# Kernel optimization log

Measured on AMD Instinct MI355X. Metric: run time of the kernel, lower is better.

Reference implementation:

```python
import jax, jax.numpy as jnp
import numpy as np

B, S, C, H = 64, 512, 256, 128
P = S  # predict_length defaults to seq_length


def _linear_init(k, fan_in, fan_out):
    bound = 1.0 / np.sqrt(fan_in)
    kw, kb = jax.random.split(k)
    w = jax.random.uniform(kw, (fan_in, fan_out), minval=-bound, maxval=bound, dtype=jnp.float32)
    b = jax.random.uniform(kb, (fan_out,), minval=-bound, maxval=bound, dtype=jnp.float32)
    return w, b


def setup_inputs() -> dict:
    key = jax.random.key(0)
    ks = jax.random.split(key, 10)
    x = jax.random.normal(ks[0], (B, S, C), dtype=jnp.float32)
    wq1, bq1 = _linear_init(ks[1], S, H)
    wk1, bk1 = _linear_init(ks[2], S, H)
    wq2, bq2 = _linear_init(ks[3], S // 2, H)
    wk2, bk2 = _linear_init(ks[4], S // 2, H)
    wq3, bq3 = _linear_init(ks[5], S // 4, H)
    wk3, bk3 = _linear_init(ks[6], S // 4, H)
    wv, bv = _linear_init(ks[7], S, S)
    wo, bo = _linear_init(ks[8], S, P)
    return dict(x=x, wq1=wq1, bq1=bq1, wk1=wk1, bk1=bk1,
                wq2=wq2, bq2=bq2, wk2=wk2, bk2=bk2,
                wq3=wq3, bq3=bq3, wk3=wk3, bk3=bk3,
                wv=wv, bv=bv, wo=wo, bo=bo)


def _channel_attn(xl, wq, bq, wk, bk):
    # xl: [b', C, L]; q,k: [b', C, H]; returns softmax channel-attention [b', C, C]
    q = xl @ wq + bq
    k = xl @ wk + bk
    scores = jnp.einsum('bch,bdh->bcd', q, k) / jnp.sqrt(jnp.asarray(H, q.dtype))
    return jax.nn.softmax(scores, axis=-1)


def reference(x, wq1, bq1, wk1, bk1, wq2, bq2, wk2, bk2, wq3, bq3, wk3, bk3, wv, bv, wo, bo):
    b, s, c = x.shape
    x1 = jnp.swapaxes(x, -2, -1)                                   # [B, C, S]
    x2 = jnp.swapaxes(x.reshape(b * 2, s // 2, c), -2, -1)          # [2B, C, S/2]
    x3 = jnp.swapaxes(x.reshape(b * 4, s // 4, c), -2, -1)          # [4B, C, S/4]
    a1 = _channel_attn(x1, wq1, bq1, wk1, bk1)                      # [B, C, C]
    a2 = _channel_attn(x2, wq2, bq2, wk2, bk2).reshape(b, 2, c, c).mean(axis=1)
    a3 = _channel_attn(x3, wq3, bq3, wk3, bk3).reshape(b, 4, c, c).mean(axis=1)
    stacked = jnp.stack([a1, a2, a3], axis=0)                       # [3, B, C, C]
    gate = jax.nn.softmax(stacked, axis=0)                          # softmax over scales
    attn = (stacked * gate).sum(axis=0)                             # gated multi-scale combine [B, C, C]
    v = x1 @ wv + bv                                                # [B, C, S]
    out = (attn @ v) @ wo + bo                                      # [B, C, P]
    return jnp.swapaxes(out, -2, -1)                                # [B, P, C]
```

## Files before the change

### kernel.cpp

```cpp
#include <hip/hip_runtime.h>
#include <hip/hip_bf16.h>


typedef __attribute__((ext_vector_type(8))) short bf16x8;
typedef __attribute__((ext_vector_type(4))) float f32x4;
typedef __attribute__((ext_vector_type(8))) unsigned short ushort8;
typedef __attribute__((ext_vector_type(4))) unsigned int uint4v;

typedef __attribute__((address_space(1))) void* as1vp;
typedef __attribute__((address_space(3))) void* as3vp;

__device__ __forceinline__ void gl2lds16(const void* g, void* l) {
  __builtin_amdgcn_global_load_lds((as1vp)(void*)g, (as3vp)l, 16, 0, 0);
}

__device__ __forceinline__ float bf2f(unsigned short u) {
  union { unsigned int i; float f; } v; v.i = ((unsigned int)u) << 16; return v.f;
}
__device__ __forceinline__ unsigned short f2bf(float f) {
  union { float f; unsigned int i; } v; v.f = f;
  unsigned int r = v.i + 0x7FFFu + ((v.i >> 16) & 1u);
  return (unsigned short)(r >> 16);
}
__device__ __forceinline__ unsigned int cvtpk(float a, float b) {
  unsigned int r;
  asm("v_cvt_pk_bf16_f32 %0, %1, %2" : "=v"(r) : "v"(a), "v"(b));
  return r;
}
__device__ __forceinline__ unsigned long long pack4pk(float a, float b, float c, float d) {
  return (unsigned long long)cvtpk(a, b) | ((unsigned long long)cvtpk(c, d) << 32);
}

__global__ void __launch_bounds__(256) tcast_all(
    const float* __restrict__ x,
    const float* __restrict__ wq1, const float* __restrict__ wk1,
    const float* __restrict__ wq2, const float* __restrict__ wk2,
    const float* __restrict__ wq3, const float* __restrict__ wk3,
    const float* __restrict__ wv, const float* __restrict__ wo,
    unsigned short* __restrict__ XT,
    unsigned short* __restrict__ W1, unsigned short* __restrict__ W2,
    unsigned short* __restrict__ W3, unsigned short* __restrict__ WVNT,
    unsigned short* __restrict__ WOT) {
  const int bid = blockIdx.x;
  const int t = threadIdx.x;
  if (bid >= 2168) {
    long i0 = (long)(bid - 2168) * 2048 + t * 8;
    f32x4 a = *(const f32x4*)(wv + i0);
    f32x4 b = *(const f32x4*)(wv + i0 + 4);
    uint4v o = {cvtpk(a[0], a[1]), cvtpk(a[2], a[3]), cvtpk(b[0], b[1]), cvtpk(b[2], b[3])};
    *(uint4v*)(WVNT + i0) = o;
    return;
  }
  __shared__ float lds[64][68];
  const float* S; unsigned short* D; int R, Cc, r0, c0, rowoff = 0;
  if (bid < 2048) {
    int bz = bid >> 5, i = bid & 31;
    S = x + (long)bz * 131072; D = XT + (long)bz * 131072;
    R = 512; Cc = 256; r0 = (i & 7) * 64; c0 = (i >> 3) * 64;
  } else {
    int wb = bid - 2048;
    if (wb < 32) {
      int m = wb >> 4, i = wb & 15;
      S = m ? wk1 : wq1; D = W1; R = 512; Cc = 128;
      r0 = (i & 7) * 64; c0 = (i >> 3) * 64; rowoff = m * 128;
    } else if (wb < 48) {
      int m = (wb - 32) >> 3, i = (wb - 32) & 7;
      S = m ? wk2 : wq2; D = W2; R = 256; Cc = 128;
      r0 = (i & 3) * 64; c0 = (i >> 2) * 64; rowoff = m * 128;
    } else if (wb < 56) {
      int m = (wb - 48) >> 2, i = (wb - 48) & 3;
      S = m ? wk3 : wq3; D = W3; R = 128; Cc = 128;
      r0 = (i & 1) * 64; c0 = (i >> 1) * 64; rowoff = m * 128;
    } else {
      int i = wb - 56; S = wo; D = WOT; R = 512; Cc = 512;
      r0 = (i & 7) * 64; c0 = (i >> 3) * 64;
    }
  }
  {
    const int row = t >> 2, cq = (t & 3) * 16;
    const float* Sp = S + (long)(r0 + row) * Cc + c0 + cq;
#pragma unroll
    for (int j = 0; j < 4; ++j)
      *(f32x4*)&lds[row][cq + j * 4] = *(const f32x4*)(Sp + j * 4);
  }
  __syncthreads();
  {
    const int rq = (t & 15) * 4, ccb = t >> 4;
#pragma unroll
    for (int j = 0; j < 4; ++j) {
      int cc = ccb + j * 16;
      *(unsigned long long*)(D + (long)(c0 + cc + rowoff) * R + r0 + rq) =
          pack4pk(lds[rq][cc], lds[rq + 1][cc], lds[rq + 2][cc], lds[rq + 3][cc]);
    }
  }
}

__global__ void __launch_bounds__(1024) projscore(
    const unsigned short* __restrict__ XT,
    const unsigned short* __restrict__ W1, const unsigned short* __restrict__ W2,
    const unsigned short* __restrict__ W3,
    const unsigned short* __restrict__ WOT, const unsigned short* __restrict__ WVNT,
    unsigned short* __restrict__ WVOT, float* __restrict__ BVO,
    const float* __restrict__ bv,
    unsigned short* __restrict__ A1F, unsigned short* __restrict__ A2F,
    unsigned short* __restrict__ A3F,
    const float* __restrict__ bq1, const float* __restrict__ bk1,
    const float* __restrict__ bq2, const float* __restrict__ bk2,
    const float* __restrict__ bq3, const float* __restrict__ bk3) {
  extern __shared__ char smem[];
  const int z = blockIdx.z;
  const int t = threadIdx.x, lane = t & 63, wid = t >> 6;

  if (z >= 464) {
    int p0 = (z - 464) * 128 + wid * 8;
    f32x4 b0 = *(const f32x4*)(bv + lane * 8);
    f32x4 b1 = *(const f32x4*)(bv + lane * 8 + 4);
#pragma unroll
    for (int i = 0; i < 8; ++i) {
      int p = p0 + i;
      bf16x8 wrow = *(const bf16x8*)(WOT + (long)p * 512 + lane * 8);
      float s = 0.0f;
#pragma unroll
      for (int j = 0; j < 4; ++j) {
        s += b0[j] * bf2f((unsigned short)wrow[j]);
        s += b1[j] * bf2f((unsigned short)wrow[4 + j]);
      }
#pragma unroll
      for (int off = 1; off < 64; off <<= 1) s += __shfl_xor(s, off, 64);
      if (lane == 0) BVO[p] = s;
    }
    return;
  }

  const int rS = t >> 3, sS = t & 7;

  if (z >= 448) {
    const int w = z - 448;
    const int m0 = (w >> 2) * 128, n0 = (w & 3) * 128;
    const unsigned short* Ab = WOT + (long)m0 * 512;
    const unsigned short* Bb = WVNT + (long)n0 * 512;
    const int wmb = (wid >> 2) * 32, wnb = (wid & 3) * 32;
    f32x4 acc[2][2] = {};
    for (int k0 = 0; k0 < 512; k0 += 64) {
      int sc = (sS ^ (rS & 7)) * 8;
      gl2lds16(Ab + (long)rS * 512 + k0 + sc, smem + t * 16);
      gl2lds16(Bb + (long)rS * 512 + k0 + sc, smem + 16384 + t * 16);
      __syncthreads();
#pragma unroll
      for (int kk = 0; kk < 2; ++kk) {
        const int slot = kk * 4 + (lane >> 4);
        bf16x8 af[2], bfr[2];
#pragma unroll
        for (int mi = 0; mi < 2; ++mi) {
          int row = wmb + mi * 16 + (lane & 15);
          af[mi] = *(const bf16x8*)(smem + row * 128 + 16 * (slot ^ (row & 7)));
        }
#pragma unroll
        for (int ni = 0; ni < 2; ++ni) {
          int row = wnb + ni * 16 + (lane & 15);
          bfr[ni] = *(const bf16x8*)(smem + 16384 + row * 128 + 16 * (slot ^ (row & 7)));
        }
#pragma unroll
        for (int mi = 0; mi < 2; ++mi)
#pragma unroll
          for (int ni = 0; ni < 2; ++ni)
            acc[mi][ni] = __builtin_amdgcn_mfma_f32_16x16x32_bf16(af[mi], bfr[ni], acc[mi][ni], 0, 0, 0);
      }
      __syncthreads();
    }
#pragma unroll
    for (int ni = 0; ni < 2; ++ni) {
      int col = n0 + wnb + ni * 16 + (lane & 15);
#pragma unroll
      for (int mi = 0; mi < 2; ++mi) {
        int rowb = m0 + wmb + mi * 16 + (lane >> 4) * 4;
#pragma unroll
        for (int r = 0; r < 4; ++r)
          WVOT[(long)(rowb + r) * 512 + col] = f2bf(acc[mi][ni][r]);
      }
    }
    return;
  }

  const unsigned short* Ab; const unsigned short* Bw; unsigned short* AF;
  const float *bq, *bk; int K; long sb;
  if (z < 64) {
    K = 512; Bw = W1; AF = A1F; sb = z; bq = bq1; bk = bk1;
    Ab = XT + (long)z * 131072;
  } else if (z < 192) {
    int u = z - 64; K = 256; Bw = W2; AF = A2F; sb = u; bq = bq2; bk = bk2;
    Ab = XT + (long)(u >> 1) * 131072 + (u & 1) * 256;
  } else {
    int u = z - 192; K = 128; Bw = W3; AF = A3F; sb = u; bq = bq3; bk = bk3;
    Ab = XT + (long)(u >> 2) * 131072 + (u & 3) * 128;
  }
  const int wmb = (wid >> 2) * 64, wnb = (wid & 3) * 64;

  auto stage = [&](int buf, int k0) {
    char* s = smem + buf * 65536;
#pragma unroll
    for (int i = 0; i < 2; ++i) {
      int row = i * 128 + rS;
      int sc = (sS ^ (row & 7)) * 8;
      gl2lds16(Ab + (long)row * 512 + k0 + sc, s + i * 16384 + t * 16);
      gl2lds16(Bw + (long)row * K + k0 + sc, s + 32768 + i * 16384 + t * 16);
    }
  };

  f32x4 acc[4][4] = {};
  const int nst = K >> 6;
  stage(0, 0);
  __syncthreads();
  int cur = 0;
  for (int j = 0; j < nst; ++j) {
    if (j + 1 < nst) stage(cur ^ 1, (j + 1) * 64);
    const char* s = smem + cur * 65536;
#pragma unroll
    for (int kk = 0; kk < 2; ++kk) {
      const int slot = kk * 4 + (lane >> 4);
      bf16x8 af[4], bfr[4];
#pragma unroll
      for (int mi = 0; mi < 4; ++mi) {
        int row = wmb + mi * 16 + (lane & 15);
        af[mi] = *(const bf16x8*)(s + row * 128 + 16 * (slot ^ (row & 7)));
      }
#pragma unroll
      for (int ni = 0; ni < 4; ++ni) {
        int row = wnb + ni * 16 + (lane & 15);
        bfr[ni] = *(const bf16x8*)(s + 32768 + row * 128 + 16 * (slot ^ (row & 7)));
      }
#pragma unroll
      for (int mi = 0; mi < 4; ++mi)
#pragma unroll
        for (int ni = 0; ni < 4; ++ni)
          acc[mi][ni] = __builtin_amdgcn_mfma_f32_16x16x32_bf16(bfr[ni], af[mi], acc[mi][ni], 0, 0, 0);
    }
    __syncthreads();
    cur ^= 1;
  }

  {
    const int chB = (wnb < 128) ? 0 : 65536;
    const float* bias = (wnb < 128) ? bq : bk;
    const int hbase = wnb & 127;
#pragma unroll
    for (int mi = 0; mi < 4; ++mi) {
      int rowm = wmb + mi * 16 + (lane & 15);
#pragma unroll
      for (int ni = 0; ni < 4; ++ni) {
        int h = hbase + ni * 16 + (lane >> 4) * 4;
        int addr = chB + (h >> 6) * 32768 + rowm * 128 +
                   16 * (((h & 63) >> 3) ^ (rowm & 7)) + (h & 7) * 2;
        *(unsigned long long*)(smem + addr) =
            pack4pk(acc[mi][ni][0] + bias[h], acc[mi][ni][1] + bias[h + 1],
                    acc[mi][ni][2] + bias[h + 2], acc[mi][ni][3] + bias[h + 3]);
      }
    }
  }
  __syncthreads();

  f32x4 acc2[16] = {};
  const int qrow = wid * 16 + (lane & 15);
#pragma unroll
  for (int kc = 0; kc < 2; ++kc)
#pragma unroll
    for (int kk = 0; kk < 2; ++kk) {
      const int slot = kk * 4 + (lane >> 4);
      bf16x8 qf = *(const bf16x8*)(smem + kc * 32768 + qrow * 128 + 16 * (slot ^ (qrow & 7)));
#pragma unroll
      for (int ni = 0; ni < 16; ++ni) {
        int krow = ni * 16 + (lane & 15);
        bf16x8 kf = *(const bf16x8*)(smem + 65536 + kc * 32768 + krow * 128 + 16 * (slot ^ (krow & 7)));
        acc2[ni] = __builtin_amdgcn_mfma_f32_16x16x32_bf16(qf, kf, acc2[ni], 0, 0, 0);
      }
    }

  const float sc = 0.088388347648318447f;
  {
    int m0idx = wid >> 2, quad = wid & 3;
    unsigned short* Of = AF + ((sb * 4 + m0idx) * 256 + quad * 64 + lane) * 64;
#pragma unroll
    for (int r = 0; r < 4; ++r) {
      float mx = -1e30f;
#pragma unroll
      for (int ni = 0; ni < 16; ++ni) mx = fmaxf(mx, acc2[ni][r]);
#pragma unroll
      for (int off = 1; off < 16; off <<= 1) mx = fmaxf(mx, __shfl_xor(mx, off, 64));
      float s = 0.0f;
      float p[16];
#pragma unroll
      for (int ni = 0; ni < 16; ++ni) {
        p[ni] = __expf((acc2[ni][r] - mx) * sc);
        s += p[ni];
      }
#pragma unroll
      for (int off = 1; off < 16; off <<= 1) s += __shfl_xor(s, off, 64);
      float inv = 1.0f / s;
      uint4v wlo = {cvtpk(p[0] * inv, p[1] * inv), cvtpk(p[2] * inv, p[3] * inv),
                    cvtpk(p[4] * inv, p[5] * inv), cvtpk(p[6] * inv, p[7] * inv)};
      uint4v whi = {cvtpk(p[8] * inv, p[9] * inv), cvtpk(p[10] * inv, p[11] * inv),
                    cvtpk(p[12] * inv, p[13] * inv), cvtpk(p[14] * inv, p[15] * inv)};
      *(uint4v*)(Of + r * 16) = wlo;
      *(uint4v*)(Of + r * 16 + 8) = whi;
    }
  }
}

__global__ void __launch_bounds__(256) gate_frag(
    const unsigned short* __restrict__ A1F, const unsigned short* __restrict__ A2F,
    const unsigned short* __restrict__ A3F, unsigned short* __restrict__ ATTN) {
  const long gid = (long)blockIdx.x * 256 + threadIdx.x;
  const long i = gid * 8;
  const int b = (int)(i >> 16);
  const int rest = (int)(i & 65535);
  ushort8 a1 = *(const ushort8*)(A1F + i);
  const long i2 = ((long)(2 * b) << 16) + rest;
  ushort8 a2a = *(const ushort8*)(A2F + i2);
  ushort8 a2b = *(const ushort8*)(A2F + i2 + 65536);
  const long i3 = ((long)(4 * b) << 16) + rest;
  ushort8 a3a = *(const ushort8*)(A3F + i3);
  ushort8 a3b = *(const ushort8*)(A3F + i3 + 65536);
  ushort8 a3c = *(const ushort8*)(A3F + i3 + 131072);
  ushort8 a3d = *(const ushort8*)(A3F + i3 + 196608);
  const int f = rest & 63;
  const int tl = (rest >> 6) & 255;
  const int m0idx = rest >> 14;
  const int quad = (tl >> 6) & 3;
  const int lane_s = tl & 63;
  const int r = f >> 4;
  const int u0 = f & 15;
  const int row = m0idx * 64 + quad * 16 + (lane_s >> 4) * 4 + r;
  unsigned short* Orow = ATTN + ((long)b << 16) + (long)row * 256 + (lane_s & 15);
#pragma unroll
  for (int j = 0; j < 8; ++j) {
    float A1 = bf2f(a1[j]);
    float A2 = 0.5f * (bf2f(a2a[j]) + bf2f(a2b[j]));
    float A3 = 0.25f * (bf2f(a3a[j]) + bf2f(a3b[j]) + bf2f(a3c[j]) + bf2f(a3d[j]));
    float m = fmaxf(A1, fmaxf(A2, A3));
    float e1 = __expf(A1 - m), e2 = __expf(A2 - m), e3 = __expf(A3 - m);
    Orow[(u0 + j) * 16] = f2bf((A1 * e1 + A2 * e2 + A3 * e3) / (e1 + e2 + e3));
  }
}

template <int F32OUT, int BIASMODE>
__global__ void __launch_bounds__(512) gemm8(
    const unsigned short* __restrict__ A, const unsigned short* __restrict__ B,
    void* __restrict__ OutV, const float* __restrict__ bias,
    int lda, int ldb, int K, long astr, long bstr, long ostr, int ldo) {
  extern __shared__ char smem[];
  const int t = threadIdx.x, lane = t & 63, wid = t >> 6;
  const int wmb = (wid >> 1) * 64, wnb = (wid & 1) * 64;
  const int m0 = blockIdx.y * 256, n0 = blockIdx.x * 128;
  const int bz = blockIdx.z;
  const unsigned short* Ab = A + (long)bz * astr + (long)m0 * lda;
  const unsigned short* Bb = B + (long)bz * bstr + (long)n0 * ldb;
  const int srow = t >> 3, ssl = t & 7;

  auto stage = [&](int buf, int k0) {
    char* s = smem + buf * 49152;
#pragma unroll
    for (int i = 0; i < 4; ++i) {
      int row = i * 64 + srow;
      gl2lds16(Ab + (long)row * lda + k0 + (ssl ^ (row & 7)) * 8, s + i * 8192 + t * 16);
    }
#pragma unroll
    for (int i = 0; i < 2; ++i) {
      int row = i * 64 + srow;
      gl2lds16(Bb + (long)row * ldb + k0 + (ssl ^ (row & 7)) * 8,
               s + 32768 + i * 8192 + t * 16);
    }
  };

  f32x4 acc[4][4] = {};
  const int nst = K >> 6;
  stage(0, 0);
  stage(1, 64);
  for (int j = 0; j < nst; ++j) {
    if (j + 1 < nst) asm volatile("s_waitcnt vmcnt(6)" ::: "memory");
    else             asm volatile("s_waitcnt vmcnt(0)" ::: "memory");
    __builtin_amdgcn_s_barrier();
    if (j + 2 < nst) stage((j + 2) % 3, (j + 2) * 64);
    const char* s = smem + (j % 3) * 49152;
#pragma unroll
    for (int kk = 0; kk < 2; ++kk) {
      const int slot = kk * 4 + (lane >> 4);
      bf16x8 af[4], bfr[4];
#pragma unroll
      for (int mi = 0; mi < 4; ++mi) {
        int row = wmb + mi * 16 + (lane & 15);
        af[mi] = *(const bf16x8*)(s + row * 128 + 16 * (slot ^ (row & 7)));
      }
#pragma unroll
      for (int ni = 0; ni < 4; ++ni) {
        int row = wnb + ni * 16 + (lane & 15);
        bfr[ni] = *(const bf16x8*)(s + 32768 + row * 128 + 16 * (slot ^ (row & 7)));
      }
#pragma unroll
      for (int mi = 0; mi < 4; ++mi)
#pragma unroll
        for (int ni = 0; ni < 4; ++ni)
          acc[mi][ni] = __builtin_amdgcn_mfma_f32_16x16x32_bf16(af[mi], bfr[ni], acc[mi][ni], 0, 0, 0);
    }
  }
#pragma unroll
  for (int mi = 0; mi < 4; ++mi) {
    int rowb = m0 + wmb + mi * 16 + (lane >> 4) * 4;
    float rb[4];
#pragma unroll
    for (int r = 0; r < 4; ++r) rb[r] = (BIASMODE == 2) ? bias[rowb + r] : 0.0f;
#pragma unroll
    for (int ni = 0; ni < 4; ++ni) {
      int col = n0 + wnb + ni * 16 + (lane & 15);
#pragma unroll
      for (int r = 0; r < 4; ++r) {
        float v = acc[mi][ni][r] + rb[r];
        if constexpr (F32OUT)
          ((float*)OutV)[(long)bz * ostr + (long)(rowb + r) * ldo + col] = v;
        else
          ((unsigned short*)OutV)[(long)bz * ostr + (long)(rowb + r) * ldo + col] = f2bf(v);
      }
    }
  }
}

extern "C" void kernel_launch(void* const* d_in, const int* in_sizes, int n_in,
                              void* d_out, int out_size, void* d_ws, size_t ws_size,
                              hipStream_t stream) {
  (void)in_sizes; (void)n_in; (void)out_size; (void)ws_size;
  const float* x   = (const float*)d_in[0];
  const float* wq1 = (const float*)d_in[1];
  const float* bq1 = (const float*)d_in[2];
  const float* wk1 = (const float*)d_in[3];
  const float* bk1 = (const float*)d_in[4];
  const float* wq2 = (const float*)d_in[5];
  const float* bq2 = (const float*)d_in[6];
  const float* wk2 = (const float*)d_in[7];
  const float* bk2 = (const float*)d_in[8];
  const float* wq3 = (const float*)d_in[9];
  const float* bq3 = (const float*)d_in[10];
  const float* wk3 = (const float*)d_in[11];
  const float* bk3 = (const float*)d_in[12];
  const float* wv  = (const float*)d_in[13];
  const float* bv  = (const float*)d_in[14];
  const float* wo  = (const float*)d_in[15];
  const float* bo  = (const float*)d_in[16];
  char* ws = (char*)d_ws;

  unsigned short* XT   = (unsigned short*)(ws + 0);
  unsigned short* WQK1 = (unsigned short*)(ws + 16777216);
  unsigned short* WQK2 = (unsigned short*)(ws + 17039360);
  unsigned short* WQK3 = (unsigned short*)(ws + 17170432);
  unsigned short* WOT  = (unsigned short*)(ws + 17235968);
  unsigned short* WVNT = (unsigned short*)(ws + 17760256);
  unsigned short* WVOT = (unsigned short*)(ws + 18284544);
  float*          BVO  = (float*)(ws + 18808832);
  unsigned short* A1F  = (unsigned short*)(ws + 18876416);
  unsigned short* A2F  = (unsigned short*)(ws + 27265024);
  unsigned short* A3F  = (unsigned short*)(ws + 44042240);
  unsigned short* ATTN = (unsigned short*)(ws + 77596672);
  unsigned short* XVT  = (unsigned short*)(ws + 18876416);

  tcast_all<<<dim3(2296), dim3(256), 0, stream>>>(
      x, wq1, wk1, wq2, wk2, wq3, wk3, wv, wo,
      XT, WQK1, WQK2, WQK3, WVNT, WOT);

  projscore<<<dim3(1, 1, 468), dim3(1024), 131072, stream>>>(
      XT, WQK1, WQK2, WQK3, WOT, WVNT, WVOT, BVO, bv,
      A1F, A2F, A3F, bq1, bk1, bq2, bk2, bq3, bk3);

  gate_frag<<<dim3(2048), dim3(256), 0, stream>>>(A1F, A2F, A3F, ATTN);

  gemm8<0, 2><<<dim3(2, 2, 64), dim3(512), 147456, stream>>>(
      WVOT, XT, XVT, BVO, 512, 512, 512, 0, 131072, 131072, 256);
  gemm8<1, 2><<<dim3(2, 2, 64), dim3(512), 147456, stream>>>(
      XVT, ATTN, d_out, bo, 256, 256, 256, 131072, 65536, 131072, 256);
}
```

Before: 91.87 us.

## Tile score GEMM as 64x64 per wave with cross-wave LDS softmax reduction

The QK^T score stage used to give each wave a 16x256 strip: one Q fragment was reused against 16 K fragments loaded from LDS. Now each wave computes a 64x64 tile, loading 4 Q and 4 K fragments per k-step, which cuts LDS reads per MFMA. Row softmax now spans four waves, so partial maxes and sums go through new LDS scratch with two extra barriers, and dynamic shared memory grows. Output stores become 8-byte writes instead of 16-byte ones.

After: 119.9 us. 30.5% more time.

```diff
diff --git a/kernel.cpp b/kernel.cpp
--- a/kernel.cpp
+++ b/kernel.cpp
@@ -259,49 +259,79 @@
   }
   __syncthreads();
 
-  f32x4 acc2[16] = {};
-  const int qrow = wid * 16 + (lane & 15);
+  const int wm2 = (wid >> 2) * 64, wn2 = (wid & 3) * 64;
+  f32x4 acc2[4][4] = {};
 #pragma unroll
   for (int kc = 0; kc < 2; ++kc)
 #pragma unroll
     for (int kk = 0; kk < 2; ++kk) {
       const int slot = kk * 4 + (lane >> 4);
-      bf16x8 qf = *(const bf16x8*)(smem + kc * 32768 + qrow * 128 + 16 * (slot ^ (qrow & 7)));
-#pragma unroll
-      for (int ni = 0; ni < 16; ++ni) {
-        int krow = ni * 16 + (lane & 15);
-        bf16x8 kf = *(const bf16x8*)(smem + 65536 + kc * 32768 + krow * 128 + 16 * (slot ^ (krow & 7)));
-        acc2[ni] = __builtin_amdgcn_mfma_f32_16x16x32_bf16(qf, kf, acc2[ni], 0, 0, 0);
-      }
-    }
-
+      bf16x8 qf[4], kf[4];
+#pragma unroll
+      for (int mi = 0; mi < 4; ++mi) {
+        int row = wm2 + mi * 16 + (lane & 15);
+        qf[mi] = *(const bf16x8*)(smem + kc * 32768 + row * 128 + 16 * (slot ^ (row & 7)));
+      }
+#pragma unroll
+      for (int ni = 0; ni < 4; ++ni) {
+        int row = wn2 + ni * 16 + (lane & 15);
+        kf[ni] = *(const bf16x8*)(smem + 65536 + kc * 32768 + row * 128 + 16 * (slot ^ (row & 7)));
+      }
+#pragma unroll
+      for (int mi = 0; mi < 4; ++mi)
+#pragma unroll
+        for (int ni = 0; ni < 4; ++ni)
+          acc2[mi][ni] = __builtin_amdgcn_mfma_f32_16x16x32_bf16(qf[mi], kf[ni], acc2[mi][ni], 0, 0, 0);
+    }
+
+  float* pmax = (float*)(smem + 131072);
+  float* psum = (float*)(smem + 135168);
   const float sc = 0.088388347648318447f;
+#pragma unroll
+  for (int mi = 0; mi < 4; ++mi)
+#pragma unroll
+    for (int r = 0; r < 4; ++r) {
+      float m = fmaxf(fmaxf(acc2[mi][0][r], acc2[mi][1][r]),
+                      fmaxf(acc2[mi][2][r], acc2[mi][3][r]));
+#pragma unroll
+      for (int off = 1; off < 16; off <<= 1) m = fmaxf(m, __shfl_xor(m, off, 64));
+      if ((lane & 15) == 0)
+        pmax[(wm2 + mi * 16 + (lane >> 4) * 4 + r) * 4 + (wid & 3)] = m;
+    }
+  __syncthreads();
+#pragma unroll
+  for (int mi = 0; mi < 4; ++mi)
+#pragma unroll
+    for (int r = 0; r < 4; ++r) {
+      int row = wm2 + mi * 16 + (lane >> 4) * 4 + r;
+      f32x4 pm = *(const f32x4*)(pmax + row * 4);
+      float M = fmaxf(fmaxf(pm[0], pm[1]), fmaxf(pm[2], pm[3]));
+      float s = 0.0f;
+#pragma unroll
+      for (int ni = 0; ni < 4; ++ni) {
+        float p = __expf((acc2[mi][ni][r] - M) * sc);
+        acc2[mi][ni][r] = p;
+        s += p;
+      }
+#pragma unroll
+      for (int off = 1; off < 16; off <<= 1) s += __shfl_xor(s, off, 64);
+      if ((lane & 15) == 0) psum[row * 4 + (wid & 3)] = s;
+    }
+  __syncthreads();
   {
-    int m0idx = wid >> 2, quad = wid & 3;
-    unsigned short* Of = AF + ((sb * 4 + m0idx) * 256 + quad * 64 + lane) * 64;
-#pragma unroll
-    for (int r = 0; r < 4; ++r) {
-      float mx = -1e30f;
-#pragma unroll
-      for (int ni = 0; ni < 16; ++ni) mx = fmaxf(mx, acc2[ni][r]);
-#pragma unroll
-      for (int off = 1; off < 16; off <<= 1) mx = fmaxf(mx, __shfl_xor(mx, off, 64));
-      float s = 0.0f;
-      float p[16];
-#pragma unroll
-      for (int ni = 0; ni < 16; ++ni) {
-        p[ni] = __expf((acc2[ni][r] - mx) * sc);
-        s += p[ni];
-      }
-#pragma unroll
-      for (int off = 1; off < 16; off <<= 1) s += __shfl_xor(s, off, 64);
-      float inv = 1.0f / s;
-      uint4v wlo = {cvtpk(p[0] * inv, p[1] * inv), cvtpk(p[2] * inv, p[3] * inv),
-                    cvtpk(p[4] * inv, p[5] * inv), cvtpk(p[6] * inv, p[7] * inv)};
-      uint4v whi = {cvtpk(p[8] * inv, p[9] * inv), cvtpk(p[10] * inv, p[11] * inv),
-                    cvtpk(p[12] * inv, p[13] * inv), cvtpk(p[14] * inv, p[15] * inv)};
-      *(uint4v*)(Of + r * 16) = wlo;
-      *(uint4v*)(Of + r * 16 + 8) = whi;
+    unsigned short* base = AF + ((sb * 4 + (wid >> 2)) * 256) * 64 + 4 * (wid & 3);
+#pragma unroll
+    for (int mi = 0; mi < 4; ++mi) {
+      unsigned short* Of = base + (mi * 64 + lane) * 64;
+#pragma unroll
+      for (int r = 0; r < 4; ++r) {
+        int row = wm2 + mi * 16 + (lane >> 4) * 4 + r;
+        f32x4 ps = *(const f32x4*)(psum + row * 4);
+        float inv = 1.0f / (ps[0] + ps[1] + ps[2] + ps[3]);
+        *(unsigned long long*)(Of + r * 16) =
+            (unsigned long long)cvtpk(acc2[mi][0][r] * inv, acc2[mi][1][r] * inv) |
+            ((unsigned long long)cvtpk(acc2[mi][2][r] * inv, acc2[mi][3][r] * inv) << 32);
+      }
     }
   }
 }
@@ -464,7 +494,7 @@
       x, wq1, wk1, wq2, wk2, wq3, wk3, wv, wo,
       XT, WQK1, WQK2, WQK3, WVNT, WOT);
 
-  projscore<<<dim3(1, 1, 468), dim3(1024), 131072, stream>>>(
+  projscore<<<dim3(1, 1, 468), dim3(1024), 139264, stream>>>(
       XT, WQK1, WQK2, WQK3, WOT, WVNT, WVOT, BVO, bv,
       A1F, A2F, A3F, bq1, bk1, bq2, bk2, bq3, bk3);
 
```
